# Kernel optimization log

Hardware: AMD Instinct MI355X
Metric: run time of the kernel (lower is better)

The kernel has to match this reference:

```python
import jax, jax.numpy as jnp
import numpy as np
from functools import partial

NUM_HEADS = 12
RATIO_ACT = 0.5   # prune_ratio_act_store
RATIO_ATTN = 0.5  # prune_ratio_attn_mat_store


def kth_mask(x, ratio):
    # torch.kthvalue semantics: threshold = k-th SMALLEST of |x| over the flat tensor
    n = x.size
    k = int(np.clip(n * ratio, 1, n))
    mag = jnp.abs(x)
    thr = jnp.sort(mag.reshape(-1))[k - 1]
    return (mag >= thr).astype(x.dtype)


def st(dense, prune):
    # straight-through: value = dense, gradient flows through `prune` path
    return jax.lax.stop_gradient(dense) + prune - jax.lax.stop_gradient(prune)


def _softmax_prune_impl(x, ratio):
    dense = jax.nn.softmax(x, axis=-1)
    mask = kth_mask(dense, ratio)
    return dense, mask * dense


@partial(jax.custom_vjp, nondiff_argnums=(1,))
def softmax_prune(x, ratio):
    return _softmax_prune_impl(x, ratio)


def _sp_fwd(x, ratio):
    dense, sparse = _softmax_prune_impl(x, ratio)
    return (dense, sparse), sparse


def _sp_bwd(ratio, A, cots):
    # custom backward uses the SPARSE probs in the softmax Jacobian; the
    # cotangent of the sparse output is ignored (matches the torch Function)
    g_dense, _ = cots
    g = A * (g_dense - jnp.sum(g_dense * A, axis=-1, keepdims=True))
    return (g,)


softmax_prune.defvjp(_sp_fwd, _sp_bwd)


def setup_inputs() -> dict:
    key = jax.random.key(0)
    ks = jax.random.split(key, 5)
    B, S, H = 8, 577, 768
    hs = jax.random.normal(ks[0], (B, S, H), dtype=jnp.float32)
    w = lambda k: jax.random.normal(k, (H, H), dtype=jnp.float32) * 0.02
    z = jnp.zeros((H,), dtype=jnp.float32)
    return {
        "hidden_states": hs,
        "Wq": w(ks[1]), "bq": z,
        "Wk": w(ks[2]), "bk": z,
        "Wv": w(ks[3]), "bv": z,
        "Wo": w(ks[4]), "bo": z,
    }


def attention_forward(hidden_states, Wq, bq, Wk, bk, Wv, bv, Wo, bo):
    B, S, H = hidden_states.shape
    nh, hd = NUM_HEADS, H // NUM_HEADS
    sg = jax.lax.stop_gradient
    lin = lambda x, W, b: x @ W + b

    # prune hidden states by global magnitude threshold
    hs_p = sg(kth_mask(hidden_states, RATIO_ACT)) * hidden_states

    q = st(lin(hidden_states, Wq, bq), lin(hs_p, Wq, bq))
    k = st(lin(hidden_states, Wk, bk), lin(hs_p, Wk, bk))
    v = st(lin(hidden_states, Wv, bv), lin(hs_p, Wv, bv))

    heads = lambda x: x.reshape(B, S, nh, hd).transpose(0, 2, 1, 3)  # [B,h,S,d]
    q, k, v = heads(q), heads(k), heads(v)

    qp = sg(kth_mask(q, RATIO_ACT)) * q
    kp = sg(kth_mask(k, RATIO_ACT)) * k

    scores = st(jnp.einsum('bhqd,bhkd->bhqk', q, k),
                jnp.einsum('bhqd,bhkd->bhqk', qp, kp))
    scores = scores / float(np.sqrt(hd))

    probs, probs_p = softmax_prune(scores, RATIO_ATTN)  # dropout rate = 0 -> identity

    vp = sg(kth_mask(v, RATIO_ACT)) * v
    ctx = st(jnp.einsum('bhqk,bhkd->bhqd', probs, v),
             jnp.einsum('bhqk,bhkd->bhqd', probs_p, vp))

    ctx = ctx.transpose(0, 2, 1, 3).reshape(B, S, H)
    ctx_p = sg(kth_mask(ctx, RATIO_ACT)) * ctx

    out = st(lin(ctx, Wo, bo), lin(ctx_p, Wo, bo))
    return out  # vis=False -> weights is None


def reference(hidden_states, Wq, bq, Wk, bk, Wv, bv, Wo, bo):
    return attention_forward(hidden_states, Wq, bq, Wk, bk, Wv, bv, Wo, bo)
```

## Files before the change

### kernel.cpp

```cpp
#include <hip/hip_runtime.h>
#include <hip/hip_bf16.h>


#define B_ 8
#define S_ 577
#define H_ 768
#define NH_ 12
#define HD_ 64
#define M_ (B_*S_)
#define MPAD 4736
#define BH_ (B_*NH_)
#define SKPAD 640
#define LTS 136

typedef __attribute__((ext_vector_type(8))) short short8;
typedef __attribute__((ext_vector_type(4))) short s16x4;
typedef __attribute__((ext_vector_type(4))) float f32x4;

__device__ inline unsigned short f2bf(float f){
    unsigned int u = __float_as_uint(f);
    u = u + 0x7fffu + ((u>>16)&1u);
    return (unsigned short)(u>>16);
}

__device__ inline void gload_lds16(const short* g, short* l){
    __builtin_amdgcn_global_load_lds((const __attribute__((address_space(1))) void*)g,
                                     (__attribute__((address_space(3))) void*)l, 16, 0, 0);
}

__global__ __launch_bounds__(256) void k_cvt(const float* __restrict__ x, short* __restrict__ y){
    int i = blockIdx.x*256 + threadIdx.x;
    if(blockIdx.x >= 1731){
        *(short8*)(y + (size_t)i*8) = (short8){};
        return;
    }
    const float4* p = (const float4*)(x + (size_t)i*8);
    float4 a = p[0], b = p[1];
    short8 v;
    v[0]=(short)f2bf(a.x); v[1]=(short)f2bf(a.y); v[2]=(short)f2bf(a.z); v[3]=(short)f2bf(a.w);
    v[4]=(short)f2bf(b.x); v[5]=(short)f2bf(b.y); v[6]=(short)f2bf(b.z); v[7]=(short)f2bf(b.w);
    *(short8*)(y + (size_t)i*8) = v;
}

__global__ __launch_bounds__(256) void k_wt(const float* __restrict__ Wq, const float* __restrict__ Wk,
                                            const float* __restrict__ Wv, const float* __restrict__ Wo,
                                            short* __restrict__ Tq, short* __restrict__ Tk,
                                            short* __restrict__ Tv, short* __restrict__ To){
    const float* W = blockIdx.z==0?Wq: blockIdx.z==1?Wk: blockIdx.z==2?Wv:Wo;
    short*       T = blockIdx.z==0?Tq: blockIdx.z==1?Tk: blockIdx.z==2?Tv:To;
    __shared__ float lds[64][65];
    int t = threadIdx.x;
    int k0 = blockIdx.x*64, n0 = blockIdx.y*64;
    for(int i=0;i<4;i++){
        int row = i*16 + (t>>4);
        int col = (t&15)*4;
        float4 v = *(const float4*)&W[(k0+row)*768 + n0 + col];
        lds[row][col]=v.x; lds[row][col+1]=v.y; lds[row][col+2]=v.z; lds[row][col+3]=v.w;
    }
    __syncthreads();
    for(int i=0;i<4;i++){
        int n = i*16 + (t>>4);
        int k4 = (t&15)*4;
        for(int j=0;j<4;j++)
            T[(n0+n)*768 + k0 + k4 + j] = (short)f2bf(lds[k4+j][n]);
    }
}

__global__ __launch_bounds__(256) void k_pad(short* __restrict__ kh, short* __restrict__ vt){
    int tid = blockIdx.x*256 + threadIdx.x;
    short8 z = {};
    if(tid < 48384){
        int row_id = tid>>3, ch = tid&7;
        int bh = row_id/63, r = row_id - bh*63;
        *(short8*)&kh[((size_t)bh*SKPAD + 577 + r)*64 + ch*8] = z;
    } else if(tid < 97536){
        int j = tid - 48384;
        int row_id = j>>3, ch = j&7;
        int bh = row_id>>6, d = row_id&63;
        *(short8*)&vt[((size_t)bh*64 + d)*SKPAD + 576 + ch*8] = z;
    }
}

__global__ __launch_bounds__(256) void k_gemm(
    const short* __restrict__ A, const short* __restrict__ T,
    const float* __restrict__ b0, const float* __restrict__ b1, const float* __restrict__ b2,
    short* __restrict__ oq, short* __restrict__ ok, short* __restrict__ ovt,
    float* __restrict__ of, int mode, int NT)
{
    __shared__ short sh[32768];
    const int t = threadIdx.x;

    const int nwg = gridDim.x;
    const int q8 = nwg>>3, r8 = nwg&7;
    const int xcd = blockIdx.x&7, cidx = blockIdx.x>>3;
    const int wg = (xcd<r8 ? xcd*(q8+1) : r8*(q8+1) + (xcd-r8)*q8) + cidx;
    const int mt = wg/NT, ntile = wg - mt*NT;
    const int m0 = mt*128, n0 = ntile*128;

    const int seg = (mode==3)? 0 : n0/768;
    const float* bias = (mode==3)? b0 : (seg==0?b0: seg==1?b1:b2);
    const int nlb = (mode==3)? n0 : n0 - seg*768;

    const int w = t>>6, lane = t&63, g = lane>>4, c = lane&15;
    const int wm = w>>1, wn = w&1;

    const int lrow = lane>>3;
    const int lcol = ((lane&7) ^ lrow) * 8;
    const short* pa = A + (size_t)(m0 + w*32 + lrow)*768 + lcol;
    const short* pb = T + (size_t)(n0 + w*32 + lrow)*768 + lcol;

    f32x4 acc[4][4] = {};

    #pragma unroll
    for(int i=0;i<4;i++){
        gload_lds16(pa + (size_t)i*8*768, &sh[(w*32+i*8)*64]);
        gload_lds16(pb + (size_t)i*8*768, &sh[8192 + (w*32+i*8)*64]);
    }
    int bb = 0;
    for(int kk=0; kk<12; kk++){
        if(kk<11){
            short* dstA = &sh[(bb^1)*16384];
            short* dstB = dstA + 8192;
            #pragma unroll
            for(int i=0;i<4;i++){
                gload_lds16(pa + (size_t)i*8*768 + (kk+1)*64, &dstA[(w*32+i*8)*64]);
                gload_lds16(pb + (size_t)i*8*768 + (kk+1)*64, &dstB[(w*32+i*8)*64]);
            }
            asm volatile("s_waitcnt vmcnt(8)" ::: "memory");
        } else {
            asm volatile("s_waitcnt vmcnt(0)" ::: "memory");
        }
        __builtin_amdgcn_s_barrier();
        asm volatile("" ::: "memory");

        const short* LA = &sh[bb*16384];
        const short* LB = LA + 8192;
        short8 af[4][2], bfv[4][2];
        #pragma unroll
        for(int mi=0; mi<4; mi++){
            int row = wm*64 + mi*16 + c;
            int rx = (row&7)<<3;
            af[mi][0] = *(const short8*)&LA[row*64 + ((g*8) ^ rx)];
            af[mi][1] = *(const short8*)&LA[row*64 + ((32 + g*8) ^ rx)];
        }
        #pragma unroll
        for(int ni=0; ni<4; ni++){
            int row = wn*64 + ni*16 + c;
            int rx = (row&7)<<3;
            bfv[ni][0] = *(const short8*)&LB[row*64 + ((g*8) ^ rx)];
            bfv[ni][1] = *(const short8*)&LB[row*64 + ((32 + g*8) ^ rx)];
        }
        #pragma unroll
        for(int mi=0; mi<4; mi++)
            #pragma unroll
            for(int ni=0; ni<4; ni++){
                acc[mi][ni] = __builtin_amdgcn_mfma_f32_16x16x32_bf16(af[mi][0], bfv[ni][0], acc[mi][ni], 0,0,0);
                acc[mi][ni] = __builtin_amdgcn_mfma_f32_16x16x32_bf16(af[mi][1], bfv[ni][1], acc[mi][ni], 0,0,0);
            }
        asm volatile("s_waitcnt lgkmcnt(0)" ::: "memory");
        __builtin_amdgcn_s_barrier();
        asm volatile("" ::: "memory");
        bb ^= 1;
    }

    if(mode==3){
        #pragma unroll
        for(int mi=0; mi<4; mi++) for(int ni=0; ni<4; ni++){
            #pragma unroll
            for(int r=0; r<4; r++){
                int m = m0 + wm*64 + mi*16 + g*4 + r;
                int n = n0 + wn*64 + ni*16 + c;
                if(m >= M_) continue;
                of[(size_t)m*768 + n] = acc[mi][ni][r] + bias[n];
            }
        }
        return;
    }

    if(seg==2){
        #pragma unroll
        for(int mi=0;mi<4;mi++)
            #pragma unroll
            for(int ni=0;ni<4;ni++){
                int nl_ = wn*64 + ni*16 + c;
                float bv = bias[nlb + nl_];
                s16x4 pk;
                #pragma unroll
                for(int r=0;r<4;r++) pk[r] = (short)f2bf(acc[mi][ni][r] + bv);
                int ml0 = wm*64 + mi*16 + g*4;
                *(s16x4*)&sh[nl_*LTS + ml0] = pk;
            }
    } else {
        #pragma unroll
        for(int mi=0;mi<4;mi++)
            #pragma unroll
            for(int ni=0;ni<4;ni++){
                int nl_ = wn*64 + ni*16 + c;
                float bv = bias[nlb + nl_];
                #pragma unroll
                for(int r=0;r<4;r++){
                    int ml = wm*64 + mi*16 + g*4 + r;
                    sh[ml*LTS + nl_] = (short)f2bf(acc[mi][ni][r] + bv);
                }
            }
    }
    __syncthreads();

    #pragma unroll
    for(int i=0;i<8;i++){
        int idx = i*256 + t;
        int rp = idx>>4, ch = idx&15;
        short8 v8 = *(const short8*)&sh[rp*LTS + ch*8];
        if(seg==2){
            int nl = nlb + rp, hh = nl>>6, dd = nl&63;
            int mg = m0 + ch*8;
            if(mg < M_){
                int b0_ = mg/S_, s0 = mg - b0_*S_;
                if(s0+7 < S_ && mg+7 < M_){
                    *(short8*)&ovt[(((size_t)b0_*NH_+hh)*HD_+dd)*SKPAD + s0] = v8;
                } else {
                    for(int j=0;j<8;j++){
                        int m=mg+j;
                        if(m<M_){ int bj=m/S_, sj=m-bj*S_;
                            ovt[(((size_t)bj*NH_+hh)*HD_+dd)*SKPAD+sj]=v8[j]; }
                    }
                }
            }
        } else {
            int m = m0 + rp;
            if(m < M_){
                int b0_ = m/S_, s0 = m - b0_*S_;
                int nl = nlb + ch*8, hh = nl>>6, dd = nl&63;
                if(seg==1) *(short8*)&ok[(((size_t)b0_*NH_+hh)*SKPAD + s0)*HD_ + dd] = v8;
                else       *(short8*)&oq[(((size_t)b0_*NH_+hh)*S_   + s0)*HD_ + dd] = v8;
            }
        }
    }
}

__global__ __launch_bounds__(256) void k_attn(
    const short* __restrict__ qh, const short* __restrict__ kh, const short* __restrict__ vt,
    short* __restrict__ ctx)
{
    __shared__ short lK[2][64*64], lV[2][64*64], lP[4*2048];
    const int t = threadIdx.x;
    const int w = t>>6, lane = t&63, g = lane>>4, c = lane&15;
    const int bh = blockIdx.x, b = bh/NH_, h = bh%NH_;
    const int q0 = blockIdx.y*128;

    #pragma unroll
    for(int i=0;i<4;i++){
        int row = i*8 + (lane>>3);
        int e8 = (lane&7)*8;
        int s = q0 + w*32 + row;
        short8 v = {};
        if(s < S_) v = *(const short8*)&qh[((size_t)bh*S_ + s)*HD_ + e8];
        *(short8*)&lP[w*2048 + row*64 + (e8 ^ ((row&7)<<3))] = v;
    }
    short8 qf[2][2];
    #pragma unroll
    for(int qi=0; qi<2; qi++)
        #pragma unroll
        for(int ks=0; ks<2; ks++)
            qf[qi][ks] = *(const short8*)&lP[w*2048 + (qi*16+c)*64 + ((ks*32+g*8) ^ ((c&7)<<3))];

    short8 ones;
    #pragma unroll
    for(int j=0;j<8;j++) ones[j] = (short)0x3F80;

    const int srow = lane>>3;
    const int sw8 = ((lane&7) ^ srow)*8;
    const short* pk0 = kh + ((size_t)bh*SKPAD + w*16 + srow)*64 + sw8;
    const short* pv0 = vt + ((size_t)bh*64 + w*16 + srow)*SKPAD + sw8;

    #pragma unroll
    for(int i=0;i<2;i++){
        gload_lds16(pk0 + i*8*64,    &lK[0][(w*16+i*8)*64]);
        gload_lds16(pv0 + i*8*SKPAD, &lV[0][(w*16+i*8)*64]);
    }

    float m_run[2][4], l_run[2][4];
    f32x4 O[2][4] = {};
    #pragma unroll
    for(int qi=0;qi<2;qi++)
        #pragma unroll
        for(int r=0;r<4;r++){ m_run[qi][r] = -3e38f; l_run[qi][r] = 0.f; }

    int bb = 0;
    for(int kt=0; kt<10; kt++){
        if(kt<9){
            const short* pk = pk0 + (kt+1)*4096;
            const short* pv = pv0 + (kt+1)*64;
            #pragma unroll
            for(int i=0;i<2;i++){
                gload_lds16(pk + i*8*64,    &lK[bb^1][(w*16+i*8)*64]);
                gload_lds16(pv + i*8*SKPAD, &lV[bb^1][(w*16+i*8)*64]);
            }
            asm volatile("s_waitcnt vmcnt(4)" ::: "memory");
        } else {
            asm volatile("s_waitcnt vmcnt(0)" ::: "memory");
        }
        __builtin_amdgcn_s_barrier();
        asm volatile("" ::: "memory");

        const short* LK = lK[bb]; const short* LV = lV[bb];

        float sv[2][4][4];
        #pragma unroll
        for(int nt=0; nt<4; nt++){
            int row = nt*16 + c;
            int rx = (row&7)<<3;
            short8 kf[2];
            kf[0] = *(const short8*)&LK[row*64 + ((g*8) ^ rx)];
            kf[1] = *(const short8*)&LK[row*64 + ((32+g*8) ^ rx)];
            #pragma unroll
            for(int qi=0; qi<2; qi++){
                f32x4 sa = {};
                sa = __builtin_amdgcn_mfma_f32_16x16x32_bf16(qf[qi][0], kf[0], sa, 0,0,0);
                sa = __builtin_amdgcn_mfma_f32_16x16x32_bf16(qf[qi][1], kf[1], sa, 0,0,0);
                #pragma unroll
                for(int r=0;r<4;r++) sv[qi][nt][r] = sa[r]*0.18033688011f;
            }
        }
        if(kt==9){
            #pragma unroll
            for(int nt=0; nt<4; nt++){
                int key = 576 + nt*16 + c;
                if(key >= S_){
                    #pragma unroll
                    for(int qi=0;qi<2;qi++)
                        #pragma unroll
                        for(int r=0;r<4;r++) sv[qi][nt][r] = -3e38f;
                }
            }
        }
        float fac[2][4];
        #pragma unroll
        for(int qi=0; qi<2; qi++)
            #pragma unroll
            for(int r=0;r<4;r++){
                float mx = fmaxf(fmaxf(sv[qi][0][r],sv[qi][1][r]),fmaxf(sv[qi][2][r],sv[qi][3][r]));
                for(int off=1; off<16; off<<=1) mx = fmaxf(mx, __shfl_xor(mx, off));
                float nm = fmaxf(m_run[qi][r], mx);
                fac[qi][r] = __builtin_amdgcn_exp2f(m_run[qi][r] - nm);
                m_run[qi][r] = nm;
            }
        #pragma unroll
        for(int qi=0; qi<2; qi++)
            #pragma unroll
            for(int nt=0; nt<4; nt++)
                #pragma unroll
                for(int r=0;r<4;r++){
                    float p = __builtin_amdgcn_exp2f(sv[qi][nt][r] - m_run[qi][r]);
                    int prow = g*4 + r;
                    lP[w*2048 + qi*1024 + prow*64 + ((nt*16 + c) ^ ((prow&7)<<3))] = (short)f2bf(p);
                }
        short8 pf[2][2];
        #pragma unroll
        for(int qi=0; qi<2; qi++)
            #pragma unroll
            for(int ks=0; ks<2; ks++)
                pf[qi][ks] = *(const short8*)&lP[w*2048 + qi*1024 + c*64 + ((ks*32+g*8) ^ ((c&7)<<3))];
        #pragma unroll
        for(int qi=0; qi<2; qi++){
            f32x4 rs = {};
            rs = __builtin_amdgcn_mfma_f32_16x16x32_bf16(pf[qi][0], ones, rs, 0,0,0);
            rs = __builtin_amdgcn_mfma_f32_16x16x32_bf16(pf[qi][1], ones, rs, 0,0,0);
            #pragma unroll
            for(int r=0;r<4;r++) l_run[qi][r] = l_run[qi][r]*fac[qi][r] + rs[r];
        }
        #pragma unroll
        for(int qi=0; qi<2; qi++)
            #pragma unroll
            for(int nt=0;nt<4;nt++)
                #pragma unroll
                for(int r=0;r<4;r++) O[qi][nt][r] *= fac[qi][r];

        #pragma unroll
        for(int nt=0; nt<4; nt++){
            int vrow = nt*16 + c;
            int rx = (vrow&7)<<3;
            short8 vf[2];
            vf[0] = *(const short8*)&LV[vrow*64 + ((g*8) ^ rx)];
            vf[1] = *(const short8*)&LV[vrow*64 + ((32+g*8) ^ rx)];
            #pragma unroll
            for(int qi=0; qi<2; qi++){
                O[qi][nt] = __builtin_amdgcn_mfma_f32_16x16x32_bf16(pf[qi][0], vf[0], O[qi][nt], 0,0,0);
                O[qi][nt] = __builtin_amdgcn_mfma_f32_16x16x32_bf16(pf[qi][1], vf[1], O[qi][nt], 0,0,0);
            }
        }
        asm volatile("s_waitcnt lgkmcnt(0)" ::: "memory");
        __builtin_amdgcn_s_barrier();
        asm volatile("" ::: "memory");
        bb ^= 1;
    }

    #pragma unroll
    for(int qi=0; qi<2; qi++)
        #pragma unroll
        for(int nt=0; nt<4; nt++)
            #pragma unroll
            for(int r=0;r<4;r++){
                int s = q0 + w*32 + qi*16 + g*4 + r;
                if(s < S_){
                    float val = O[qi][nt][r] / l_run[qi][r];
                    ctx[((size_t)b*S_ + s)*H_ + h*HD_ + nt*16 + c] = (short)f2bf(val);
                }
            }
}

extern "C" void kernel_launch(void* const* d_in, const int* in_sizes, int n_in,
                              void* d_out, int out_size, void* d_ws, size_t ws_size,
                              hipStream_t stream)
{
    const float* hs = (const float*)d_in[0];
    const float* Wq = (const float*)d_in[1];
    const float* bq = (const float*)d_in[2];
    const float* Wk = (const float*)d_in[3];
    const float* bk = (const float*)d_in[4];
    const float* Wv = (const float*)d_in[5];
    const float* bv = (const float*)d_in[6];
    const float* Wo = (const float*)d_in[7];
    const float* bo = (const float*)d_in[8];
    float* out = (float*)d_out;

    char* ws = (char*)d_ws;
    short* abf = (short*)(ws);
    short* ctx = abf;
    short* wqt = (short*)(ws + 7274496);
    short* wkt = (short*)(ws + 7274496 + 1179648);
    short* wvt = (short*)(ws + 7274496 + 2*1179648);
    short* wot = (short*)(ws + 7274496 + 3*1179648);
    short* qh  = (short*)(ws + 11993088);
    short* kh  = (short*)(ws + 19083264);
    short* vt  = (short*)(ws + 26947584);

    k_cvt<<<1776, 256, 0, stream>>>(hs, abf);
    k_wt<<<dim3(12,12,4), 256, 0, stream>>>(Wq,Wk,Wv,Wo, wqt,wkt,wvt,wot);
    k_pad<<<381, 256, 0, stream>>>(kh, vt);
    k_gemm<<<666, 256, 0, stream>>>(abf, wqt, bq,bk,bv, qh,kh,vt, nullptr, 0, 18);
    k_attn<<<dim3(96,5), 256, 0, stream>>>(qh, kh, vt, ctx);
    k_gemm<<<222, 256, 0, stream>>>(ctx, wot, bo,bo,bo, nullptr,nullptr,nullptr, out, 3, 6);
}
```

Measured before the change: 104.4 us.

## Fuse prep kernels, use 512-thread GEMM blocks, add MFMA priority hints

Merges the hidden-state conversion, weight transpose and pad-zeroing kernels into one launch to cut launch overhead. The GEMM moves from 256 to 512 threads per block, so each of the 8 waves computes a 32x64 sub-tile instead of 64x64. This lowers per-wave register pressure and adds more waves to hide latency. s_setprio hints are wrapped around the MFMA sections in the GEMM and attention kernels. The cost is less register-level reuse per wave and more LDS fragment reads per MFMA.

```diff
diff --git a/kernel.cpp b/kernel.cpp
--- a/kernel.cpp
+++ b/kernel.cpp
@@ -28,60 +28,62 @@
                                      (__attribute__((address_space(3))) void*)l, 16, 0, 0);
 }
 
-__global__ __launch_bounds__(256) void k_cvt(const float* __restrict__ x, short* __restrict__ y){
-    int i = blockIdx.x*256 + threadIdx.x;
-    if(blockIdx.x >= 1731){
-        *(short8*)(y + (size_t)i*8) = (short8){};
-        return;
-    }
-    const float4* p = (const float4*)(x + (size_t)i*8);
-    float4 a = p[0], b = p[1];
-    short8 v;
-    v[0]=(short)f2bf(a.x); v[1]=(short)f2bf(a.y); v[2]=(short)f2bf(a.z); v[3]=(short)f2bf(a.w);
-    v[4]=(short)f2bf(b.x); v[5]=(short)f2bf(b.y); v[6]=(short)f2bf(b.z); v[7]=(short)f2bf(b.w);
-    *(short8*)(y + (size_t)i*8) = v;
-}
-
-__global__ __launch_bounds__(256) void k_wt(const float* __restrict__ Wq, const float* __restrict__ Wk,
-                                            const float* __restrict__ Wv, const float* __restrict__ Wo,
-                                            short* __restrict__ Tq, short* __restrict__ Tk,
-                                            short* __restrict__ Tv, short* __restrict__ To){
-    const float* W = blockIdx.z==0?Wq: blockIdx.z==1?Wk: blockIdx.z==2?Wv:Wo;
-    short*       T = blockIdx.z==0?Tq: blockIdx.z==1?Tk: blockIdx.z==2?Tv:To;
-    __shared__ float lds[64][65];
-    int t = threadIdx.x;
-    int k0 = blockIdx.x*64, n0 = blockIdx.y*64;
-    for(int i=0;i<4;i++){
-        int row = i*16 + (t>>4);
-        int col = (t&15)*4;
-        float4 v = *(const float4*)&W[(k0+row)*768 + n0 + col];
-        lds[row][col]=v.x; lds[row][col+1]=v.y; lds[row][col+2]=v.z; lds[row][col+3]=v.w;
-    }
-    __syncthreads();
-    for(int i=0;i<4;i++){
-        int n = i*16 + (t>>4);
-        int k4 = (t&15)*4;
-        for(int j=0;j<4;j++)
-            T[(n0+n)*768 + k0 + k4 + j] = (short)f2bf(lds[k4+j][n]);
-    }
-}
-
-__global__ __launch_bounds__(256) void k_pad(short* __restrict__ kh, short* __restrict__ vt){
-    int tid = blockIdx.x*256 + threadIdx.x;
-    short8 z = {};
-    if(tid < 48384){
-        int row_id = tid>>3, ch = tid&7;
-        int bh = row_id/63, r = row_id - bh*63;
-        *(short8*)&kh[((size_t)bh*SKPAD + 577 + r)*64 + ch*8] = z;
-    } else if(tid < 97536){
-        int j = tid - 48384;
-        int row_id = j>>3, ch = j&7;
-        int bh = row_id>>6, d = row_id&63;
-        *(short8*)&vt[((size_t)bh*64 + d)*SKPAD + 576 + ch*8] = z;
-    }
-}
-
-__global__ __launch_bounds__(256) void k_gemm(
+__global__ __launch_bounds__(256) void k_prep(
+    const float* __restrict__ hs, short* __restrict__ abf,
+    const float* __restrict__ Wq, const float* __restrict__ Wk,
+    const float* __restrict__ Wv, const float* __restrict__ Wo,
+    short* __restrict__ Tq, short* __restrict__ Tk,
+    short* __restrict__ Tv, short* __restrict__ To,
+    short* __restrict__ kh, short* __restrict__ vt)
+{
+    const int bid = blockIdx.x, t = threadIdx.x;
+    if(bid < 1776){
+        int i = bid*256 + t;
+        if(bid >= 1731){ *(short8*)(abf + (size_t)i*8) = (short8){}; return; }
+        const float4* p = (const float4*)(hs + (size_t)i*8);
+        float4 a = p[0], b = p[1];
+        short8 v;
+        v[0]=(short)f2bf(a.x); v[1]=(short)f2bf(a.y); v[2]=(short)f2bf(a.z); v[3]=(short)f2bf(a.w);
+        v[4]=(short)f2bf(b.x); v[5]=(short)f2bf(b.y); v[6]=(short)f2bf(b.z); v[7]=(short)f2bf(b.w);
+        *(short8*)(abf + (size_t)i*8) = v;
+    } else if(bid < 2352){
+        int zidx = bid - 1776;
+        int z = zidx & 3, rem = zidx >> 2;
+        int kx = rem % 12, ny = rem / 12;
+        const float* W = z==0?Wq: z==1?Wk: z==2?Wv:Wo;
+        short*       T = z==0?Tq: z==1?Tk: z==2?Tv:To;
+        __shared__ float lds[64][65];
+        int k0 = kx*64, n0 = ny*64;
+        for(int i=0;i<4;i++){
+            int row = i*16 + (t>>4);
+            int col = (t&15)*4;
+            float4 v = *(const float4*)&W[(k0+row)*768 + n0 + col];
+            lds[row][col]=v.x; lds[row][col+1]=v.y; lds[row][col+2]=v.z; lds[row][col+3]=v.w;
+        }
+        __syncthreads();
+        for(int i=0;i<4;i++){
+            int n = i*16 + (t>>4);
+            int k4 = (t&15)*4;
+            for(int j=0;j<4;j++)
+                T[(n0+n)*768 + k0 + k4 + j] = (short)f2bf(lds[k4+j][n]);
+        }
+    } else {
+        int tid = (bid-2352)*256 + t;
+        short8 z = {};
+        if(tid < 48384){
+            int row_id = tid>>3, ch = tid&7;
+            int bh = row_id/63, r = row_id - bh*63;
+            *(short8*)&kh[((size_t)bh*SKPAD + 577 + r)*64 + ch*8] = z;
+        } else if(tid < 97536){
+            int j = tid - 48384;
+            int row_id = j>>3, ch = j&7;
+            int bh = row_id>>6, d = row_id&63;
+            *(short8*)&vt[((size_t)bh*64 + d)*SKPAD + 576 + ch*8] = z;
+        }
+    }
+}
+
+__global__ __launch_bounds__(512) void k_gemm(
     const short* __restrict__ A, const short* __restrict__ T,
     const float* __restrict__ b0, const float* __restrict__ b1, const float* __restrict__ b2,
     short* __restrict__ oq, short* __restrict__ ok, short* __restrict__ ovt,
@@ -106,15 +108,15 @@
 
     const int lrow = lane>>3;
     const int lcol = ((lane&7) ^ lrow) * 8;
-    const short* pa = A + (size_t)(m0 + w*32 + lrow)*768 + lcol;
-    const short* pb = T + (size_t)(n0 + w*32 + lrow)*768 + lcol;
-
-    f32x4 acc[4][4] = {};
-
-    #pragma unroll
-    for(int i=0;i<4;i++){
-        gload_lds16(pa + (size_t)i*8*768, &sh[(w*32+i*8)*64]);
-        gload_lds16(pb + (size_t)i*8*768, &sh[8192 + (w*32+i*8)*64]);
+    const short* pa = A + (size_t)(m0 + w*8 + lrow)*768 + lcol;
+    const short* pb = T + (size_t)(n0 + w*8 + lrow)*768 + lcol;
+
+    f32x4 acc[2][4] = {};
+
+    #pragma unroll
+    for(int i=0;i<2;i++){
+        gload_lds16(pa + (size_t)(i*64)*768, &sh[(i*64 + w*8)*64]);
+        gload_lds16(pb + (size_t)(i*64)*768, &sh[8192 + (i*64 + w*8)*64]);
     }
     int bb = 0;
     for(int kk=0; kk<12; kk++){
@@ -122,11 +124,11 @@
             short* dstA = &sh[(bb^1)*16384];
             short* dstB = dstA + 8192;
             #pragma unroll
-            for(int i=0;i<4;i++){
-                gload_lds16(pa + (size_t)i*8*768 + (kk+1)*64, &dstA[(w*32+i*8)*64]);
-                gload_lds16(pb + (size_t)i*8*768 + (kk+1)*64, &dstB[(w*32+i*8)*64]);
-            }
-            asm volatile("s_waitcnt vmcnt(8)" ::: "memory");
+            for(int i=0;i<2;i++){
+                gload_lds16(pa + (size_t)(i*64)*768 + (kk+1)*64, &dstA[(i*64 + w*8)*64]);
+                gload_lds16(pb + (size_t)(i*64)*768 + (kk+1)*64, &dstB[(i*64 + w*8)*64]);
+            }
+            asm volatile("s_waitcnt vmcnt(4)" ::: "memory");
         } else {
             asm volatile("s_waitcnt vmcnt(0)" ::: "memory");
         }
@@ -135,10 +137,10 @@
 
         const short* LA = &sh[bb*16384];
         const short* LB = LA + 8192;
-        short8 af[4][2], bfv[4][2];
-        #pragma unroll
-        for(int mi=0; mi<4; mi++){
-            int row = wm*64 + mi*16 + c;
+        short8 af[2][2], bfv[4][2];
+        #pragma unroll
+        for(int mi=0; mi<2; mi++){
+            int row = wm*32 + mi*16 + c;
             int rx = (row&7)<<3;
             af[mi][0] = *(const short8*)&LA[row*64 + ((g*8) ^ rx)];
             af[mi][1] = *(const short8*)&LA[row*64 + ((32 + g*8) ^ rx)];
@@ -150,13 +152,15 @@
             bfv[ni][0] = *(const short8*)&LB[row*64 + ((g*8) ^ rx)];
             bfv[ni][1] = *(const short8*)&LB[row*64 + ((32 + g*8) ^ rx)];
         }
-        #pragma unroll
-        for(int mi=0; mi<4; mi++)
+        __builtin_amdgcn_s_setprio(1);
+        #pragma unroll
+        for(int mi=0; mi<2; mi++)
             #pragma unroll
             for(int ni=0; ni<4; ni++){
                 acc[mi][ni] = __builtin_amdgcn_mfma_f32_16x16x32_bf16(af[mi][0], bfv[ni][0], acc[mi][ni], 0,0,0);
                 acc[mi][ni] = __builtin_amdgcn_mfma_f32_16x16x32_bf16(af[mi][1], bfv[ni][1], acc[mi][ni], 0,0,0);
             }
+        __builtin_amdgcn_s_setprio(0);
         asm volatile("s_waitcnt lgkmcnt(0)" ::: "memory");
         __builtin_amdgcn_s_barrier();
         asm volatile("" ::: "memory");
@@ -165,10 +169,10 @@
 
     if(mode==3){
         #pragma unroll
-        for(int mi=0; mi<4; mi++) for(int ni=0; ni<4; ni++){
+        for(int mi=0; mi<2; mi++) for(int ni=0; ni<4; ni++){
             #pragma unroll
             for(int r=0; r<4; r++){
-                int m = m0 + wm*64 + mi*16 + g*4 + r;
+                int m = m0 + wm*32 + mi*16 + g*4 + r;
                 int n = n0 + wn*64 + ni*16 + c;
                 if(m >= M_) continue;
                 of[(size_t)m*768 + n] = acc[mi][ni][r] + bias[n];
@@ -179,7 +183,7 @@
 
     if(seg==2){
         #pragma unroll
-        for(int mi=0;mi<4;mi++)
+        for(int mi=0;mi<2;mi++)
             #pragma unroll
             for(int ni=0;ni<4;ni++){
                 int nl_ = wn*64 + ni*16 + c;
@@ -187,19 +191,19 @@
                 s16x4 pk;
                 #pragma unroll
                 for(int r=0;r<4;r++) pk[r] = (short)f2bf(acc[mi][ni][r] + bv);
-                int ml0 = wm*64 + mi*16 + g*4;
+                int ml0 = wm*32 + mi*16 + g*4;
                 *(s16x4*)&sh[nl_*LTS + ml0] = pk;
             }
     } else {
         #pragma unroll
-        for(int mi=0;mi<4;mi++)
+        for(int mi=0;mi<2;mi++)
             #pragma unroll
             for(int ni=0;ni<4;ni++){
                 int nl_ = wn*64 + ni*16 + c;
                 float bv = bias[nlb + nl_];
                 #pragma unroll
                 for(int r=0;r<4;r++){
-                    int ml = wm*64 + mi*16 + g*4 + r;
+                    int ml = wm*32 + mi*16 + g*4 + r;
                     sh[ml*LTS + nl_] = (short)f2bf(acc[mi][ni][r] + bv);
                 }
             }
@@ -207,8 +211,8 @@
     __syncthreads();
 
     #pragma unroll
-    for(int i=0;i<8;i++){
-        int idx = i*256 + t;
+    for(int i=0;i<4;i++){
+        int idx = i*512 + t;
         int rp = idx>>4, ch = idx&15;
         short8 v8 = *(const short8*)&sh[rp*LTS + ch*8];
         if(seg==2){
@@ -313,6 +317,7 @@
             short8 kf[2];
             kf[0] = *(const short8*)&LK[row*64 + ((g*8) ^ rx)];
             kf[1] = *(const short8*)&LK[row*64 + ((32+g*8) ^ rx)];
+            __builtin_amdgcn_s_setprio(1);
             #pragma unroll
             for(int qi=0; qi<2; qi++){
                 f32x4 sa = {};
@@ -321,6 +326,7 @@
                 #pragma unroll
                 for(int r=0;r<4;r++) sv[qi][nt][r] = sa[r]*0.18033688011f;
             }
+            __builtin_amdgcn_s_setprio(0);
         }
         if(kt==9){
             #pragma unroll
@@ -361,6 +367,7 @@
             #pragma unroll
             for(int ks=0; ks<2; ks++)
                 pf[qi][ks] = *(const short8*)&lP[w*2048 + qi*1024 + c*64 + ((ks*32+g*8) ^ ((c&7)<<3))];
+        __builtin_amdgcn_s_setprio(1);
         #pragma unroll
         for(int qi=0; qi<2; qi++){
             f32x4 rs = {};
@@ -369,6 +376,7 @@
             #pragma unroll
             for(int r=0;r<4;r++) l_run[qi][r] = l_run[qi][r]*fac[qi][r] + rs[r];
         }
+        __builtin_amdgcn_s_setprio(0);
         #pragma unroll
         for(int qi=0; qi<2; qi++)
             #pragma unroll
@@ -376,6 +384,7 @@
                 #pragma unroll
                 for(int r=0;r<4;r++) O[qi][nt][r] *= fac[qi][r];
 
+        __builtin_amdgcn_s_setprio(1);
         #pragma unroll
         for(int nt=0; nt<4; nt++){
             int vrow = nt*16 + c;
@@ -389,6 +398,7 @@
                 O[qi][nt] = __builtin_amdgcn_mfma_f32_16x16x32_bf16(pf[qi][1], vf[1], O[qi][nt], 0,0,0);
             }
         }
+        __builtin_amdgcn_s_setprio(0);
         asm volatile("s_waitcnt lgkmcnt(0)" ::: "memory");
         __builtin_amdgcn_s_barrier();
         asm volatile("" ::: "memory");
@@ -435,10 +445,8 @@
     short* kh  = (short*)(ws + 19083264);
     short* vt  = (short*)(ws + 26947584);
 
-    k_cvt<<<1776, 256, 0, stream>>>(hs, abf);
-    k_wt<<<dim3(12,12,4), 256, 0, stream>>>(Wq,Wk,Wv,Wo, wqt,wkt,wvt,wot);
-    k_pad<<<381, 256, 0, stream>>>(kh, vt);
-    k_gemm<<<666, 256, 0, stream>>>(abf, wqt, bq,bk,bv, qh,kh,vt, nullptr, 0, 18);
+    k_prep<<<2733, 256, 0, stream>>>(hs, abf, Wq,Wk,Wv,Wo, wqt,wkt,wvt,wot, kh, vt);
+    k_gemm<<<666, 512, 0, stream>>>(abf, wqt, bq,bk,bv, qh,kh,vt, nullptr, 0, 18);
     k_attn<<<dim3(96,5), 256, 0, stream>>>(qh, kh, vt, ctx);
-    k_gemm<<<222, 256, 0, stream>>>(ctx, wot, bo,bo,bo, nullptr,nullptr,nullptr, out, 3, 6);
-}
+    k_gemm<<<222, 512, 0, stream>>>(ctx, wot, bo,bo,bo, nullptr,nullptr,nullptr, out, 3, 6);
+}
```

New measurement: 90.36 us, median of 2. 13.4% less time.

## Merge prep kernels into one launch and transpose attention MFMA layout

Applied to the files above, without the earlier changes.

Folds the three preprocessing kernels (input bf16 conversion, weight transpose, K/V padding zeroing) into a single launch to cut launch overhead. In the attention kernel the MFMA operands are swapped so each lane holds a whole query row's scores. That turns row max and row sum into mostly in-register reductions with two cross-lane shuffles, replaces the ones-vector MFMA row-sum, and allows packed 4-element P writes and ctx stores. It also adds s_setprio around the MFMA sections. The new tail-mask condition (nt*16+g*4+r >= 1) must match the swapped layout exactly, so key masking is a correctness risk.

```diff
diff --git a/kernel.cpp b/kernel.cpp
--- a/kernel.cpp
+++ b/kernel.cpp
@@ -28,56 +28,58 @@
                                      (__attribute__((address_space(3))) void*)l, 16, 0, 0);
 }
 
-__global__ __launch_bounds__(256) void k_cvt(const float* __restrict__ x, short* __restrict__ y){
-    int i = blockIdx.x*256 + threadIdx.x;
-    if(blockIdx.x >= 1731){
-        *(short8*)(y + (size_t)i*8) = (short8){};
-        return;
-    }
-    const float4* p = (const float4*)(x + (size_t)i*8);
-    float4 a = p[0], b = p[1];
-    short8 v;
-    v[0]=(short)f2bf(a.x); v[1]=(short)f2bf(a.y); v[2]=(short)f2bf(a.z); v[3]=(short)f2bf(a.w);
-    v[4]=(short)f2bf(b.x); v[5]=(short)f2bf(b.y); v[6]=(short)f2bf(b.z); v[7]=(short)f2bf(b.w);
-    *(short8*)(y + (size_t)i*8) = v;
-}
-
-__global__ __launch_bounds__(256) void k_wt(const float* __restrict__ Wq, const float* __restrict__ Wk,
-                                            const float* __restrict__ Wv, const float* __restrict__ Wo,
-                                            short* __restrict__ Tq, short* __restrict__ Tk,
-                                            short* __restrict__ Tv, short* __restrict__ To){
-    const float* W = blockIdx.z==0?Wq: blockIdx.z==1?Wk: blockIdx.z==2?Wv:Wo;
-    short*       T = blockIdx.z==0?Tq: blockIdx.z==1?Tk: blockIdx.z==2?Tv:To;
-    __shared__ float lds[64][65];
-    int t = threadIdx.x;
-    int k0 = blockIdx.x*64, n0 = blockIdx.y*64;
-    for(int i=0;i<4;i++){
-        int row = i*16 + (t>>4);
-        int col = (t&15)*4;
-        float4 v = *(const float4*)&W[(k0+row)*768 + n0 + col];
-        lds[row][col]=v.x; lds[row][col+1]=v.y; lds[row][col+2]=v.z; lds[row][col+3]=v.w;
-    }
-    __syncthreads();
-    for(int i=0;i<4;i++){
-        int n = i*16 + (t>>4);
-        int k4 = (t&15)*4;
-        for(int j=0;j<4;j++)
-            T[(n0+n)*768 + k0 + k4 + j] = (short)f2bf(lds[k4+j][n]);
-    }
-}
-
-__global__ __launch_bounds__(256) void k_pad(short* __restrict__ kh, short* __restrict__ vt){
-    int tid = blockIdx.x*256 + threadIdx.x;
-    short8 z = {};
-    if(tid < 48384){
-        int row_id = tid>>3, ch = tid&7;
-        int bh = row_id/63, r = row_id - bh*63;
-        *(short8*)&kh[((size_t)bh*SKPAD + 577 + r)*64 + ch*8] = z;
-    } else if(tid < 97536){
-        int j = tid - 48384;
-        int row_id = j>>3, ch = j&7;
-        int bh = row_id>>6, d = row_id&63;
-        *(short8*)&vt[((size_t)bh*64 + d)*SKPAD + 576 + ch*8] = z;
+__global__ __launch_bounds__(256) void k_prep(
+    const float* __restrict__ hs, short* __restrict__ abf,
+    const float* __restrict__ Wq, const float* __restrict__ Wk,
+    const float* __restrict__ Wv, const float* __restrict__ Wo,
+    short* __restrict__ Tq, short* __restrict__ Tk,
+    short* __restrict__ Tv, short* __restrict__ To,
+    short* __restrict__ kh, short* __restrict__ vt)
+{
+    const int bid = blockIdx.x, t = threadIdx.x;
+    if(bid < 1776){
+        int i = bid*256 + t;
+        if(bid >= 1731){ *(short8*)(abf + (size_t)i*8) = (short8){}; return; }
+        const float4* p = (const float4*)(hs + (size_t)i*8);
+        float4 a = p[0], b = p[1];
+        short8 v;
+        v[0]=(short)f2bf(a.x); v[1]=(short)f2bf(a.y); v[2]=(short)f2bf(a.z); v[3]=(short)f2bf(a.w);
+        v[4]=(short)f2bf(b.x); v[5]=(short)f2bf(b.y); v[6]=(short)f2bf(b.z); v[7]=(short)f2bf(b.w);
+        *(short8*)(abf + (size_t)i*8) = v;
+    } else if(bid < 2352){
+        int zidx = bid - 1776;
+        int z = zidx & 3, rem = zidx >> 2;
+        int kx = rem % 12, ny = rem / 12;
+        const float* W = z==0?Wq: z==1?Wk: z==2?Wv:Wo;
+        short*       T = z==0?Tq: z==1?Tk: z==2?Tv:To;
+        __shared__ float lds[64][65];
+        int k0 = kx*64, n0 = ny*64;
+        for(int i=0;i<4;i++){
+            int row = i*16 + (t>>4);
+            int col = (t&15)*4;
+            float4 v = *(const float4*)&W[(k0+row)*768 + n0 + col];
+            lds[row][col]=v.x; lds[row][col+1]=v.y; lds[row][col+2]=v.z; lds[row][col+3]=v.w;
+        }
+        __syncthreads();
+        for(int i=0;i<4;i++){
+            int n = i*16 + (t>>4);
+            int k4 = (t&15)*4;
+            for(int j=0;j<4;j++)
+                T[(n0+n)*768 + k0 + k4 + j] = (short)f2bf(lds[k4+j][n]);
+        }
+    } else {
+        int tid = (bid-2352)*256 + t;
+        short8 z = {};
+        if(tid < 48384){
+            int row_id = tid>>3, ch = tid&7;
+            int bh = row_id/63, r = row_id - bh*63;
+            *(short8*)&kh[((size_t)bh*SKPAD + 577 + r)*64 + ch*8] = z;
+        } else if(tid < 97536){
+            int j = tid - 48384;
+            int row_id = j>>3, ch = j&7;
+            int bh = row_id>>6, d = row_id&63;
+            *(short8*)&vt[((size_t)bh*64 + d)*SKPAD + 576 + ch*8] = z;
+        }
     }
 }
 
@@ -264,10 +266,6 @@
         for(int ks=0; ks<2; ks++)
             qf[qi][ks] = *(const short8*)&lP[w*2048 + (qi*16+c)*64 + ((ks*32+g*8) ^ ((c&7)<<3))];
 
-    short8 ones;
-    #pragma unroll
-    for(int j=0;j<8;j++) ones[j] = (short)0x3F80;
-
     const int srow = lane>>3;
     const int sw8 = ((lane&7) ^ srow)*8;
     const short* pk0 = kh + ((size_t)bh*SKPAD + w*16 + srow)*64 + sw8;
@@ -279,12 +277,10 @@
         gload_lds16(pv0 + i*8*SKPAD, &lV[0][(w*16+i*8)*64]);
     }
 
-    float m_run[2][4], l_run[2][4];
+    float m_run[2], l_run[2];
     f32x4 O[2][4] = {};
     #pragma unroll
-    for(int qi=0;qi<2;qi++)
-        #pragma unroll
-        for(int r=0;r<4;r++){ m_run[qi][r] = -3e38f; l_run[qi][r] = 0.f; }
+    for(int qi=0;qi<2;qi++){ m_run[qi] = -3e38f; l_run[qi] = 0.f; }
 
     int bb = 0;
     for(int kt=0; kt<10; kt++){
@@ -313,69 +309,69 @@
             short8 kf[2];
             kf[0] = *(const short8*)&LK[row*64 + ((g*8) ^ rx)];
             kf[1] = *(const short8*)&LK[row*64 + ((32+g*8) ^ rx)];
+            __builtin_amdgcn_s_setprio(1);
             #pragma unroll
             for(int qi=0; qi<2; qi++){
                 f32x4 sa = {};
-                sa = __builtin_amdgcn_mfma_f32_16x16x32_bf16(qf[qi][0], kf[0], sa, 0,0,0);
-                sa = __builtin_amdgcn_mfma_f32_16x16x32_bf16(qf[qi][1], kf[1], sa, 0,0,0);
+                sa = __builtin_amdgcn_mfma_f32_16x16x32_bf16(kf[0], qf[qi][0], sa, 0,0,0);
+                sa = __builtin_amdgcn_mfma_f32_16x16x32_bf16(kf[1], qf[qi][1], sa, 0,0,0);
                 #pragma unroll
                 for(int r=0;r<4;r++) sv[qi][nt][r] = sa[r]*0.18033688011f;
             }
+            __builtin_amdgcn_s_setprio(0);
         }
         if(kt==9){
             #pragma unroll
+            for(int nt=0; nt<4; nt++)
+                #pragma unroll
+                for(int r=0;r<4;r++){
+                    if(nt*16 + g*4 + r >= 1){
+                        sv[0][nt][r] = -3e38f;
+                        sv[1][nt][r] = -3e38f;
+                    }
+                }
+        }
+        #pragma unroll
+        for(int qi=0; qi<2; qi++){
+            float mx = sv[qi][0][0];
+            #pragma unroll
+            for(int nt=0; nt<4; nt++)
+                #pragma unroll
+                for(int r=0;r<4;r++) mx = fmaxf(mx, sv[qi][nt][r]);
+            mx = fmaxf(mx, __shfl_xor(mx, 16));
+            mx = fmaxf(mx, __shfl_xor(mx, 32));
+            float nm = fmaxf(m_run[qi], mx);
+            float fac = __builtin_amdgcn_exp2f(m_run[qi] - nm);
+            m_run[qi] = nm;
+            float ts = 0.f;
+            #pragma unroll
             for(int nt=0; nt<4; nt++){
-                int key = 576 + nt*16 + c;
-                if(key >= S_){
-                    #pragma unroll
-                    for(int qi=0;qi<2;qi++)
-                        #pragma unroll
-                        for(int r=0;r<4;r++) sv[qi][nt][r] = -3e38f;
+                s16x4 pk;
+                #pragma unroll
+                for(int r=0;r<4;r++){
+                    float p = __builtin_amdgcn_exp2f(sv[qi][nt][r] - nm);
+                    ts += p;
+                    pk[r] = (short)f2bf(p);
                 }
-            }
-        }
-        float fac[2][4];
+                int slot = 2*nt + (g>>1);
+                *(s16x4*)&lP[w*2048 + qi*1024 + c*64 + ((slot ^ (c&7))<<3) + ((g&1)<<2)] = pk;
+            }
+            ts += __shfl_xor(ts, 16);
+            ts += __shfl_xor(ts, 32);
+            l_run[qi] = l_run[qi]*fac + ts;
+            #pragma unroll
+            for(int nt=0;nt<4;nt++)
+                #pragma unroll
+                for(int r=0;r<4;r++) O[qi][nt][r] *= fac;
+        }
+        short8 pf[2][2];
         #pragma unroll
         for(int qi=0; qi<2; qi++)
             #pragma unroll
-            for(int r=0;r<4;r++){
-                float mx = fmaxf(fmaxf(sv[qi][0][r],sv[qi][1][r]),fmaxf(sv[qi][2][r],sv[qi][3][r]));
-                for(int off=1; off<16; off<<=1) mx = fmaxf(mx, __shfl_xor(mx, off));
-                float nm = fmaxf(m_run[qi][r], mx);
-                fac[qi][r] = __builtin_amdgcn_exp2f(m_run[qi][r] - nm);
-                m_run[qi][r] = nm;
-            }
-        #pragma unroll
-        for(int qi=0; qi<2; qi++)
-            #pragma unroll
-            for(int nt=0; nt<4; nt++)
-                #pragma unroll
-                for(int r=0;r<4;r++){
-                    float p = __builtin_amdgcn_exp2f(sv[qi][nt][r] - m_run[qi][r]);
-                    int prow = g*4 + r;
-                    lP[w*2048 + qi*1024 + prow*64 + ((nt*16 + c) ^ ((prow&7)<<3))] = (short)f2bf(p);
-                }
-        short8 pf[2][2];
-        #pragma unroll
-        for(int qi=0; qi<2; qi++)
-            #pragma unroll
             for(int ks=0; ks<2; ks++)
-                pf[qi][ks] = *(const short8*)&lP[w*2048 + qi*1024 + c*64 + ((ks*32+g*8) ^ ((c&7)<<3))];
-        #pragma unroll
-        for(int qi=0; qi<2; qi++){
-            f32x4 rs = {};
-            rs = __builtin_amdgcn_mfma_f32_16x16x32_bf16(pf[qi][0], ones, rs, 0,0,0);
-            rs = __builtin_amdgcn_mfma_f32_16x16x32_bf16(pf[qi][1], ones, rs, 0,0,0);
-            #pragma unroll
-            for(int r=0;r<4;r++) l_run[qi][r] = l_run[qi][r]*fac[qi][r] + rs[r];
-        }
-        #pragma unroll
-        for(int qi=0; qi<2; qi++)
-            #pragma unroll
-            for(int nt=0;nt<4;nt++)
-                #pragma unroll
-                for(int r=0;r<4;r++) O[qi][nt][r] *= fac[qi][r];
-
+                pf[qi][ks] = *(const short8*)&lP[w*2048 + qi*1024 + c*64 + (((4*ks+g) ^ (c&7))<<3)];
+
+        __builtin_amdgcn_s_setprio(1);
         #pragma unroll
         for(int nt=0; nt<4; nt++){
             int vrow = nt*16 + c;
@@ -385,10 +381,11 @@
             vf[1] = *(const short8*)&LV[vrow*64 + ((32+g*8) ^ rx)];
             #pragma unroll
             for(int qi=0; qi<2; qi++){
-                O[qi][nt] = __builtin_amdgcn_mfma_f32_16x16x32_bf16(pf[qi][0], vf[0], O[qi][nt], 0,0,0);
-                O[qi][nt] = __builtin_amdgcn_mfma_f32_16x16x32_bf16(pf[qi][1], vf[1], O[qi][nt], 0,0,0);
-            }
-        }
+                O[qi][nt] = __builtin_amdgcn_mfma_f32_16x16x32_bf16(vf[0], pf[qi][0], O[qi][nt], 0,0,0);
+                O[qi][nt] = __builtin_amdgcn_mfma_f32_16x16x32_bf16(vf[1], pf[qi][1], O[qi][nt], 0,0,0);
+            }
+        }
+        __builtin_amdgcn_s_setprio(0);
         asm volatile("s_waitcnt lgkmcnt(0)" ::: "memory");
         __builtin_amdgcn_s_barrier();
         asm volatile("" ::: "memory");
@@ -396,17 +393,19 @@
     }
 
     #pragma unroll
-    for(int qi=0; qi<2; qi++)
-        #pragma unroll
-        for(int nt=0; nt<4; nt++)
-            #pragma unroll
-            for(int r=0;r<4;r++){
-                int s = q0 + w*32 + qi*16 + g*4 + r;
-                if(s < S_){
-                    float val = O[qi][nt][r] / l_run[qi][r];
-                    ctx[((size_t)b*S_ + s)*H_ + h*HD_ + nt*16 + c] = (short)f2bf(val);
-                }
-            }
+    for(int qi=0; qi<2; qi++){
+        float rinv = 1.0f / l_run[qi];
+        int s = q0 + w*32 + qi*16 + c;
+        if(s < S_){
+            #pragma unroll
+            for(int nt=0; nt<4; nt++){
+                s16x4 ov;
+                #pragma unroll
+                for(int r=0;r<4;r++) ov[r] = (short)f2bf(O[qi][nt][r] * rinv);
+                *(s16x4*)&ctx[((size_t)b*S_ + s)*H_ + h*HD_ + nt*16 + g*4] = ov;
+            }
+        }
+    }
 }
 
 extern "C" void kernel_launch(void* const* d_in, const int* in_sizes, int n_in,
@@ -435,9 +434,7 @@
     short* kh  = (short*)(ws + 19083264);
     short* vt  = (short*)(ws + 26947584);
 
-    k_cvt<<<1776, 256, 0, stream>>>(hs, abf);
-    k_wt<<<dim3(12,12,4), 256, 0, stream>>>(Wq,Wk,Wv,Wo, wqt,wkt,wvt,wot);
-    k_pad<<<381, 256, 0, stream>>>(kh, vt);
+    k_prep<<<2733, 256, 0, stream>>>(hs, abf, Wq,Wk,Wv,Wo, wqt,wkt,wvt,wot, kh, vt);
     k_gemm<<<666, 256, 0, stream>>>(abf, wqt, bq,bk,bv, qh,kh,vt, nullptr, 0, 18);
     k_attn<<<dim3(96,5), 256, 0, stream>>>(qh, kh, vt, ctx);
     k_gemm<<<222, 256, 0, stream>>>(ctx, wot, bo,bo,bo, nullptr,nullptr,nullptr, out, 3, 6);
```

New measurement: 93.23 us. 1.12x faster.
